# Optimization experiments

Hardware: AMD Instinct MI355X
Metric: run time of the kernel (lower is better)

Reference implementation:

```python
import jax, jax.numpy as jnp
import numpy as np

NUM_CARDS = 40
NUM_SUITS = 4
SIDE_SUIT_LEN = 9
NUM_ACTIONS = 2 * NUM_CARDS + 1  # 81 (use_signals=True)
NUM_TRICKS = 10


def setup_inputs() -> dict:
    key = jax.random.key(0)
    ks = jax.random.split(key, 8)
    B, A, D_in, D_q = 16384, 40, 4096, 256
    backbone_embed = jax.random.normal(ks[0], (B, D_in), dtype=jnp.float32)
    rank = jax.random.randint(ks[1], (B, A), -1, SIDE_SUIT_LEN)
    # guarantee at least one valid action per row (slot 0)
    rank = rank.at[:, 0].set(jnp.maximum(rank[:, 0], 0))
    suit = jax.random.randint(ks[2], (B, A), 0, NUM_SUITS + 1)  # suit==NUM_SUITS -> no-signal action
    valid_actions = jnp.stack([rank, suit], axis=-1)
    phase = jax.random.randint(ks[3], (B,), 0, 2)
    trick = jax.random.randint(ks[4], (B,), 0, NUM_TRICKS)
    # params
    Wq = jax.random.normal(ks[5], (D_in, D_q), dtype=jnp.float32) / np.sqrt(D_in).astype(np.float32)
    bq = jnp.zeros((D_q,), jnp.float32)
    key_table = jax.random.normal(ks[6], (NUM_ACTIONS, D_q), dtype=jnp.float32)
    ln_gamma = jnp.ones((D_q,), jnp.float32)
    ln_beta = jnp.zeros((D_q,), jnp.float32)
    # signal_prior == 'lin': p_signal = 2 / (num_tricks_left + 1)
    num_left = NUM_TRICKS - jnp.arange(NUM_TRICKS, dtype=jnp.float32)
    p_signal = 2.0 / (num_left + 1.0)
    return dict(backbone_embed=backbone_embed, valid_actions=valid_actions, phase=phase,
                trick=trick, Wq=Wq, bq=bq, key_table=key_table, ln_gamma=ln_gamma,
                ln_beta=ln_beta, p_signal=p_signal)


def reference(backbone_embed, valid_actions, phase, trick, Wq, bq, key_table, ln_gamma, ln_beta, p_signal):
    D_q = Wq.shape[1]
    rank = valid_actions[..., 0]          # (B, A)
    suit = valid_actions[..., 1]          # (B, A)
    aidx = phase[:, None] * NUM_CARDS + suit * SIDE_SUIT_LEN + rank
    aidx = jnp.where(rank == -1, -1, jnp.where(suit == NUM_SUITS, 2 * NUM_CARDS, aidx))
    # PaddedEmbed: shift by 1, row 0 is the zero padding row for idx == -1
    table = jnp.concatenate([jnp.zeros((1, D_q), key_table.dtype), key_table], axis=0)
    k = table[aidx + 1]                   # (B, A, D_q)
    # LayerNorm over last dim
    mu = k.mean(axis=-1, keepdims=True)
    var = k.var(axis=-1, keepdims=True)
    k = (k - mu) * jax.lax.rsqrt(var + 1e-5) * ln_gamma + ln_beta
    q = backbone_embed @ Wq + bq          # (B, D_q)
    attn = jnp.einsum('bq,baq->ba', q, k) / jnp.sqrt(jnp.float32(D_q))
    attn = jnp.where(rank == -1, -jnp.inf, attn)
    # no-signal bias on action 0 during signal phase
    n_valid = (rank != -1).sum(axis=-1).astype(jnp.float32)
    ps = p_signal[trick]
    w = jnp.log(jnp.maximum((1.0 - ps) / ps * (n_valid - 1.0), 1e-5))
    w = jnp.where(n_valid == 1.0, 0.0, w)
    attn = attn.at[:, 0].add(jnp.where(phase == 1, w, 0.0))
    return jax.nn.log_softmax(attn, axis=-1)
```

## Files before the change

### kernel.cpp

```cpp
#include <hip/hip_runtime.h>
#include <hip/hip_bf16.h>
#include <math.h>


typedef _Float16 half8_t __attribute__((ext_vector_type(8)));
typedef float    f32x4_t __attribute__((ext_vector_type(4)));

#define NUM_B 16384
#define D_IN  4096
#define D_Q   256
#define N_ACT 40

__device__ __forceinline__ half8_t cvt8(const float4 a, const float4 b) {
  half8_t h;
  h[0] = (_Float16)a.x; h[1] = (_Float16)a.y; h[2] = (_Float16)a.z; h[3] = (_Float16)a.w;
  h[4] = (_Float16)b.x; h[5] = (_Float16)b.y; h[6] = (_Float16)b.z; h[7] = (_Float16)b.w;
  return h;
}
__device__ __forceinline__ void gl_lds16f(const float* g, float* l) {
  __builtin_amdgcn_global_load_lds(
      (const __attribute__((address_space(1))) void*)g,
      (__attribute__((address_space(3))) void*)l, 16, 0, 0);
}
__device__ __forceinline__ void gl_lds16h(const _Float16* g, _Float16* l) {
  __builtin_amdgcn_global_load_lds(
      (const __attribute__((address_space(1))) void*)g,
      (__attribute__((address_space(3))) void*)l, 16, 0, 0);
}

__global__ __launch_bounds__(256) void ln_table_k(const float* __restrict__ kt,
                                                  const float* __restrict__ gamma,
                                                  const float* __restrict__ beta,
                                                  const float* __restrict__ bq,
                                                  float* __restrict__ out,
                                                  float* __restrict__ bqk) {
  __shared__ float red[8];
  __shared__ float red2[4];
  const int t = threadIdx.x, r = blockIdx.x;
  float v = kt[r * 256 + t];
  float s = v, sq = v * v;
#pragma unroll
  for (int off = 1; off < 64; off <<= 1) {
    s  += __shfl_xor(s, off);
    sq += __shfl_xor(sq, off);
  }
  if ((t & 63) == 0) { red[t >> 6] = s; red[4 + (t >> 6)] = sq; }
  __syncthreads();
  s  = red[0] + red[1] + red[2] + red[3];
  sq = red[4] + red[5] + red[6] + red[7];
  const float mu  = s * (1.0f / 256.0f);
  const float var = sq * (1.0f / 256.0f) - mu * mu;
  const float inv = 1.0f / sqrtf(var + 1e-5f);
  const float o = (v - mu) * inv * gamma[t] + beta[t];
  out[r * 256 + t] = o;
  float p = o * bq[t];
#pragma unroll
  for (int off = 1; off < 64; off <<= 1) p += __shfl_xor(p, off);
  if ((t & 63) == 0) red2[t >> 6] = p;
  __syncthreads();
  if (t == 0) bqk[r] = red2[0] + red2[1] + red2[2] + red2[3];
}

__global__ __launch_bounds__(256) void wk_gemm_k(const float* __restrict__ Wq,
                                                 const float* __restrict__ tbl,
                                                 _Float16* __restrict__ Bf) {
  const int lane = threadIdx.x & 63, w = threadIdx.x >> 6;
  const int wm = w >> 1, wn = w & 1;
  const int m0 = blockIdx.x * 64 + wm * 32;
  const int n0 = wn * 64;
  const int fr = lane & 15, fg = lane >> 4;
  f32x4_t acc[2][4] = {};
  for (int k0 = 0; k0 < 256; k0 += 32) {
    half8_t af[2], bf[4];
#pragma unroll
    for (int i = 0; i < 2; ++i) {
      const float* p = Wq + (size_t)(m0 + i * 16 + fr) * D_Q + k0 + fg * 8;
      af[i] = cvt8(*(const float4*)p, *(const float4*)(p + 4));
    }
#pragma unroll
    for (int j = 0; j < 4; ++j) {
      const int n = n0 + j * 16 + fr;
      if (n < 81) {
        const float* p = tbl + (size_t)n * D_Q + k0 + fg * 8;
        bf[j] = cvt8(*(const float4*)p, *(const float4*)(p + 4));
      } else {
        bf[j] = (half8_t)(_Float16)0.0f;
      }
    }
#pragma unroll
    for (int i = 0; i < 2; ++i)
#pragma unroll
      for (int j = 0; j < 4; ++j)
        acc[i][j] = __builtin_amdgcn_mfma_f32_16x16x32_f16(af[i], bf[j], acc[i][j], 0, 0, 0);
  }
#pragma unroll
  for (int i = 0; i < 2; ++i)
#pragma unroll
    for (int j = 0; j < 4; ++j)
#pragma unroll
      for (int r = 0; r < 4; ++r) {
        const int k = m0 + i * 16 + fg * 4 + r;
        const int n = n0 + j * 16 + fr;
        const int kt32 = k >> 5, fgb = (k >> 3) & 3, e = k & 7;
        const int jg = n >> 4, frb = n & 15;
        Bf[(((size_t)kt32 * 8 + jg) * 64 + fgb * 16 + frb) * 8 + e] =
            (_Float16)acc[i][j][r];
      }
}

__global__ __launch_bounds__(512) void gemm_part_k(const float* __restrict__ A,
                                                   const _Float16* __restrict__ Bf,
                                                   float* __restrict__ part) {
  __shared__ __align__(16) char smem[65536];
  float*    Afs = (float*)smem;
  _Float16* Bls = (_Float16*)(smem + 32768);

  const int t = threadIdx.x, lane = t & 63, w = t >> 6;
  const int fr = lane & 15, fg = lane >> 4;
  const int ks = blockIdx.y;
  const size_t row0 = (size_t)blockIdx.x * 64;
  const int k0 = ks * 2048;

#define STAGE(T, P)                                                           \
  do {                                                                        \
    float* abase = Afs + (P)*4096;                                            \
    _Float16* bbase = Bls + (P)*8192;                                         \
    _Pragma("unroll") for (int q_ = 0; q_ < 4; ++q_) {                        \
      const int id_ = w * 4 + q_;                                             \
      if (id_ < 16) {                                                         \
        const int r_ = id_ * 4 + (lane >> 4);                                 \
        gl_lds16f(A + (size_t)(row0 + r_) * D_IN + k0 + (T)*64 +              \
                      (((lane & 15) ^ (r_ & 7)) << 2),                        \
                  abase + id_ * 256);                                         \
      } else {                                                                \
        const int ib_ = id_ - 16;                                             \
        gl_lds16h(Bf + ((size_t)(ks * 32 + (T))) * 8192 + ib_ * 512 + lane * 8, \
                  bbase + ib_ * 512);                                         \
      }                                                                       \
    }                                                                         \
  } while (0)

  const int wm = w >> 2, wn = w & 3;
  int aoff[2][2][2], boff[2][2];
#pragma unroll
  for (int i = 0; i < 2; ++i)
#pragma unroll
    for (int c = 0; c < 2; ++c)
#pragma unroll
      for (int h = 0; h < 2; ++h)
        aoff[i][c][h] = (wm * 32 + i * 16 + fr) * 64 +
                        (((c * 8 + fg * 2 + h) ^ (fr & 7)) * 4);
#pragma unroll
  for (int c = 0; c < 2; ++c)
#pragma unroll
    for (int j = 0; j < 2; ++j)
      boff[c][j] = c * 4096 + (wn * 2 + j) * 512 + lane * 8;

  f32x4_t acc[2][2] = {};

  STAGE(0, 0);
  for (int kt = 0; kt < 32; ++kt) {
    if (kt < 31) STAGE(kt + 1, (kt + 1) & 1);
    __builtin_amdgcn_sched_barrier(0);
    if (kt < 31) asm volatile("s_waitcnt vmcnt(4)" ::: "memory");
    else         asm volatile("s_waitcnt vmcnt(0)" ::: "memory");
    __builtin_amdgcn_s_barrier();
    __builtin_amdgcn_sched_barrier(0);

    const float*    Ap = Afs + (kt & 1) * 4096;
    const _Float16* Bp = Bls + (kt & 1) * 8192;
#pragma unroll
    for (int c = 0; c < 2; ++c) {
      half8_t bfv[2];
#pragma unroll
      for (int j = 0; j < 2; ++j) bfv[j] = *(const half8_t*)(Bp + boff[c][j]);
#pragma unroll
      for (int i = 0; i < 2; ++i) {
        const float4 x0 = *(const float4*)(Ap + aoff[i][c][0]);
        const float4 x1 = *(const float4*)(Ap + aoff[i][c][1]);
        const half8_t af = cvt8(x0, x1);
#pragma unroll
        for (int j = 0; j < 2; ++j)
          acc[i][j] = __builtin_amdgcn_mfma_f32_16x16x32_f16(af, bfv[j], acc[i][j], 0, 0, 0);
      }
    }
    asm volatile("s_waitcnt lgkmcnt(0)" ::: "memory");
    __builtin_amdgcn_s_barrier();
    __builtin_amdgcn_sched_barrier(0);
  }
#undef STAGE

  float* pb = part + ((size_t)ks * NUM_B + row0) * 128;
#pragma unroll
  for (int i = 0; i < 2; ++i)
#pragma unroll
    for (int j = 0; j < 2; ++j) {
      const int col = wn * 32 + j * 16 + fr;
#pragma unroll
      for (int r = 0; r < 4; ++r)
        pb[(size_t)(wm * 32 + i * 16 + fg * 4 + r) * 128 + col] = acc[i][j][r];
    }
}

__global__ __launch_bounds__(256) void softmax_k(const float* __restrict__ part,
                                                 const float* __restrict__ bqk,
                                                 const int* __restrict__ va,
                                                 const int* __restrict__ phase,
                                                 const int* __restrict__ trick,
                                                 const float* __restrict__ psig,
                                                 float* __restrict__ out) {
  const int t = threadIdx.x;
  const int lane = t & 63, w = t >> 6;
  const int b = blockIdx.x * 4 + w;

  float sx = 0.f, sy = 0.f;
#pragma unroll
  for (int ks = 0; ks < 2; ++ks) {
    const float2 v = *(const float2*)&part[((size_t)ks * NUM_B + b) * 128 + lane * 2];
    sx += v.x; sy += v.y;
  }

  int rank = -1, suit = 0;
  if (lane < N_ACT) {
    rank = va[((size_t)b * N_ACT + lane) * 2];
    suit = va[((size_t)b * N_ACT + lane) * 2 + 1];
  }
  const int ph = phase[b];
  const bool valid = (rank >= 0);
  const int aidx = valid ? (suit == 4 ? 80 : ph * 40 + suit * 9 + rank) : -1;
  const int nvalid = __popcll(__ballot(valid));

  const int srcl = valid ? (aidx >> 1) : 0;
  const float v0 = __shfl(sx, srcl);
  const float v1 = __shfl(sy, srcl);

  float attn_l = -INFINITY;
  if (valid) attn_l = (((aidx & 1) ? v1 : v0) + bqk[aidx]) * 0.0625f;

  if (ph == 1 && lane == 0) {
    const float ps = psig[trick[b]];
    const float nv = (float)nvalid;
    const float wv = (nv == 1.0f) ? 0.0f
                                  : logf(fmaxf((1.0f - ps) / ps * (nv - 1.0f), 1e-5f));
    attn_l += wv;
  }

  float m = attn_l;
#pragma unroll
  for (int off = 1; off < 64; off <<= 1) m = fmaxf(m, __shfl_xor(m, off));
  const float e = expf(attn_l - m);
  float ssum = e;
#pragma unroll
  for (int off = 1; off < 64; off <<= 1) ssum += __shfl_xor(ssum, off);
  const float o = attn_l - m - logf(ssum);
  if (lane < N_ACT) out[(size_t)b * N_ACT + lane] = valid ? o : -3.0e38f;
}

extern "C" void kernel_launch(void* const* d_in, const int* in_sizes, int n_in,
                              void* d_out, int out_size, void* d_ws, size_t ws_size,
                              hipStream_t stream) {
  const float* backbone = (const float*)d_in[0];
  const int*   va       = (const int*)d_in[1];
  const int*   phase    = (const int*)d_in[2];
  const int*   trick    = (const int*)d_in[3];
  const float* Wq       = (const float*)d_in[4];
  const float* bq       = (const float*)d_in[5];
  const float* keytab   = (const float*)d_in[6];
  const float* gamma    = (const float*)d_in[7];
  const float* beta     = (const float*)d_in[8];
  const float* psig     = (const float*)d_in[9];
  float* out = (float*)d_out;

  char* ws = (char*)d_ws;
  _Float16* Bf   = (_Float16*)ws;
  float* tableLN = (float*)(ws + (1u << 20));
  float* bqk     = (float*)(ws + (1u << 20) + (128u << 10));
  float* part    = (float*)(ws + (2u << 20));

  ln_table_k<<<dim3(81), 256, 0, stream>>>(keytab, gamma, beta, bq, tableLN, bqk);
  wk_gemm_k<<<dim3(64), 256, 0, stream>>>(Wq, tableLN, Bf);
  gemm_part_k<<<dim3(NUM_B / 64, 2), 512, 0, stream>>>(backbone, Bf, part);
  softmax_k<<<dim3(NUM_B / 4), 256, 0, stream>>>(part, bqk, va, phase, trick,
                                                 psig, out);
}
```

Baseline: 89.68 us.

## Enlarge GEMM row tile to 128 and split K four ways

The query-key GEMM block now covers 128 rows instead of 64, and the K dimension is split into four partitions instead of two, keeping the same block count. A is staged 64 k-columns at a time, loaded in two halves across alternating iterations, while B is staged 32 k at a time. Each warp now owns a 32x64 output tile with 8 accumulators, so each staged B tile serves twice as many rows. The cost is double the partial-sum buffer traffic written by the GEMM and read by softmax, more LDS per block, and more complex vmcnt bookkeeping.

Result: slower. 105.2 us (+17.3%).

```diff
diff --git a/kernel.cpp b/kernel.cpp
--- a/kernel.cpp
+++ b/kernel.cpp
@@ -111,91 +111,100 @@
 __global__ __launch_bounds__(512) void gemm_part_k(const float* __restrict__ A,
                                                    const _Float16* __restrict__ Bf,
                                                    float* __restrict__ part) {
-  __shared__ __align__(16) char smem[65536];
+  __shared__ __align__(16) char smem[81920];
   float*    Afs = (float*)smem;
-  _Float16* Bls = (_Float16*)(smem + 32768);
+  _Float16* Bls = (_Float16*)(smem + 65536);
 
   const int t = threadIdx.x, lane = t & 63, w = t >> 6;
   const int fr = lane & 15, fg = lane >> 4;
   const int ks = blockIdx.y;
-  const size_t row0 = (size_t)blockIdx.x * 64;
-  const int k0 = ks * 2048;
-
-#define STAGE(T, P)                                                           \
+  const size_t row0 = (size_t)blockIdx.x * 128;
+  const int k0 = ks * 1024;
+
+#define STAGE_B(TB)                                                           \
   do {                                                                        \
-    float* abase = Afs + (P)*4096;                                            \
-    _Float16* bbase = Bls + (P)*8192;                                         \
-    _Pragma("unroll") for (int q_ = 0; q_ < 4; ++q_) {                        \
-      const int id_ = w * 4 + q_;                                             \
-      if (id_ < 16) {                                                         \
-        const int r_ = id_ * 4 + (lane >> 4);                                 \
-        gl_lds16f(A + (size_t)(row0 + r_) * D_IN + k0 + (T)*64 +              \
-                      (((lane & 15) ^ (r_ & 7)) << 2),                        \
-                  abase + id_ * 256);                                         \
-      } else {                                                                \
-        const int ib_ = id_ - 16;                                             \
-        gl_lds16h(Bf + ((size_t)(ks * 32 + (T))) * 8192 + ib_ * 512 + lane * 8, \
-                  bbase + ib_ * 512);                                         \
-      }                                                                       \
+    gl_lds16h(Bf + ((size_t)(ks * 32 + (TB))) * 4096 + w * 512 + lane * 8,    \
+              Bls + ((TB)&1) * 4096 + w * 512);                               \
+  } while (0)
+#define STAGE_A(SU, HF)                                                       \
+  do {                                                                        \
+    float* abase = Afs + ((SU)&1) * 8192;                                     \
+    _Pragma("unroll") for (int q_ = 0; q_ < 2; ++q_) {                        \
+      const int id_ = (HF)*16 + w * 2 + q_;                                   \
+      const int r_ = id_ * 4 + (lane >> 4);                                   \
+      gl_lds16f(A + (size_t)(row0 + r_) * D_IN + k0 + (SU)*64 +               \
+                    (((lane & 15) ^ (r_ & 7)) << 2),                          \
+                abase + id_ * 256);                                           \
     }                                                                         \
   } while (0)
 
-  const int wm = w >> 2, wn = w & 3;
-  int aoff[2][2][2], boff[2][2];
+  int aoff[2][2][2];
 #pragma unroll
   for (int i = 0; i < 2; ++i)
 #pragma unroll
-    for (int c = 0; c < 2; ++c)
-#pragma unroll
-      for (int h = 0; h < 2; ++h)
-        aoff[i][c][h] = (wm * 32 + i * 16 + fr) * 64 +
-                        (((c * 8 + fg * 2 + h) ^ (fr & 7)) * 4);
-#pragma unroll
-  for (int c = 0; c < 2; ++c)
-#pragma unroll
-    for (int j = 0; j < 2; ++j)
-      boff[c][j] = c * 4096 + (wn * 2 + j) * 512 + lane * 8;
-
-  f32x4_t acc[2][2] = {};
-
-  STAGE(0, 0);
+    for (int kh = 0; kh < 2; ++kh)
+#pragma unroll
+      for (int h = 0; h < 2; ++h) {
+        const int R = (w >> 1) * 32 + i * 16 + fr;
+        aoff[i][kh][h] = R * 64 + (((kh * 8 + fg * 2 + h) ^ (R & 7)) << 2);
+      }
+  const int wm = w >> 1, wn = w & 1;
+  int boff[4];
+#pragma unroll
+  for (int j = 0; j < 4; ++j) boff[j] = (wn * 4 + j) * 512 + lane * 8;
+
+  f32x4_t acc[2][4] = {};
+
+  STAGE_B(0);
+  STAGE_A(0, 0);
+  STAGE_A(0, 1);
+
   for (int kt = 0; kt < 32; ++kt) {
-    if (kt < 31) STAGE(kt + 1, (kt + 1) & 1);
+    if (kt < 31) STAGE_B(kt + 1);
+    if (kt < 30) {
+      if ((kt & 1) == 0) STAGE_A((kt >> 1) + 1, 0);
+      else               STAGE_A((kt >> 1) + 1, 1);
+    }
     __builtin_amdgcn_sched_barrier(0);
-    if (kt < 31) asm volatile("s_waitcnt vmcnt(4)" ::: "memory");
-    else         asm volatile("s_waitcnt vmcnt(0)" ::: "memory");
+    if (kt < 30) {
+      if ((kt & 1) == 0) asm volatile("s_waitcnt vmcnt(3)" ::: "memory");
+      else               asm volatile("s_waitcnt vmcnt(5)" ::: "memory");
+    } else if (kt == 30) {
+      asm volatile("s_waitcnt vmcnt(1)" ::: "memory");
+    } else {
+      asm volatile("s_waitcnt vmcnt(0)" ::: "memory");
+    }
     __builtin_amdgcn_s_barrier();
     __builtin_amdgcn_sched_barrier(0);
 
-    const float*    Ap = Afs + (kt & 1) * 4096;
-    const _Float16* Bp = Bls + (kt & 1) * 8192;
-#pragma unroll
-    for (int c = 0; c < 2; ++c) {
-      half8_t bfv[2];
-#pragma unroll
-      for (int j = 0; j < 2; ++j) bfv[j] = *(const half8_t*)(Bp + boff[c][j]);
-#pragma unroll
-      for (int i = 0; i < 2; ++i) {
-        const float4 x0 = *(const float4*)(Ap + aoff[i][c][0]);
-        const float4 x1 = *(const float4*)(Ap + aoff[i][c][1]);
-        const half8_t af = cvt8(x0, x1);
-#pragma unroll
-        for (int j = 0; j < 2; ++j)
-          acc[i][j] = __builtin_amdgcn_mfma_f32_16x16x32_f16(af, bfv[j], acc[i][j], 0, 0, 0);
-      }
+    const float*    Ap = Afs + ((kt >> 1) & 1) * 8192;
+    const _Float16* Bp = Bls + (kt & 1) * 4096;
+    const int kh = kt & 1;
+    half8_t bfv[4];
+#pragma unroll
+    for (int j = 0; j < 4; ++j) bfv[j] = *(const half8_t*)(Bp + boff[j]);
+#pragma unroll
+    for (int i = 0; i < 2; ++i) {
+      const float4 x0 = *(const float4*)(Ap + aoff[i][kh][0]);
+      const float4 x1 = *(const float4*)(Ap + aoff[i][kh][1]);
+      const half8_t af = cvt8(x0, x1);
+#pragma unroll
+      for (int j = 0; j < 4; ++j)
+        acc[i][j] = __builtin_amdgcn_mfma_f32_16x16x32_f16(af, bfv[j], acc[i][j], 0, 0, 0);
     }
     asm volatile("s_waitcnt lgkmcnt(0)" ::: "memory");
     __builtin_amdgcn_s_barrier();
     __builtin_amdgcn_sched_barrier(0);
   }
-#undef STAGE
+#undef STAGE_A
+#undef STAGE_B
 
   float* pb = part + ((size_t)ks * NUM_B + row0) * 128;
 #pragma unroll
   for (int i = 0; i < 2; ++i)
 #pragma unroll
-    for (int j = 0; j < 2; ++j) {
-      const int col = wn * 32 + j * 16 + fr;
+    for (int j = 0; j < 4; ++j) {
+      const int col = wn * 64 + j * 16 + fr;
 #pragma unroll
       for (int r = 0; r < 4; ++r)
         pb[(size_t)(wm * 32 + i * 16 + fg * 4 + r) * 128 + col] = acc[i][j][r];
@@ -215,7 +224,7 @@
 
   float sx = 0.f, sy = 0.f;
 #pragma unroll
-  for (int ks = 0; ks < 2; ++ks) {
+  for (int ks = 0; ks < 4; ++ks) {
     const float2 v = *(const float2*)&part[((size_t)ks * NUM_B + b) * 128 + lane * 2];
     sx += v.x; sy += v.y;
   }
@@ -279,7 +288,7 @@
 
   ln_table_k<<<dim3(81), 256, 0, stream>>>(keytab, gamma, beta, bq, tableLN, bqk);
   wk_gemm_k<<<dim3(64), 256, 0, stream>>>(Wq, tableLN, Bf);
-  gemm_part_k<<<dim3(NUM_B / 64, 2), 512, 0, stream>>>(backbone, Bf, part);
+  gemm_part_k<<<dim3(NUM_B / 128, 4), 512, 0, stream>>>(backbone, Bf, part);
   softmax_k<<<dim3(NUM_B / 4), 256, 0, stream>>>(part, bqk, va, phase, trick,
                                                  psig, out);
 }
```

## Use single-buffered 256-thread GEMM blocks with 4-way split-K for higher occupancy

Applied to the files above, without the earlier changes.

Reworks the main GEMM from 512-thread double-buffered blocks with 2-way split-K into 256-thread single-buffered blocks with 4-way split-K. Each warp now computes a 32x64 tile, and LDS per block drops to 32KB, so more blocks can be resident per CU. The aim is to hide memory latency through occupancy rather than explicit prefetch. In exchange, loads no longer overlap compute inside a block and two __syncthreads run per k-step. The partial-sum buffer also doubles, so the softmax kernel reads four partials instead of two.

Result: slower. 103.6 us (+15.5%).

```diff
diff --git a/kernel.cpp b/kernel.cpp
--- a/kernel.cpp
+++ b/kernel.cpp
@@ -108,85 +108,79 @@
       }
 }
 
-__global__ __launch_bounds__(512) void gemm_part_k(const float* __restrict__ A,
-                                                   const _Float16* __restrict__ Bf,
-                                                   float* __restrict__ part) {
-  __shared__ __align__(16) char smem[65536];
+__global__ __launch_bounds__(256, 4) void gemm_part_k(const float* __restrict__ A,
+                                                      const _Float16* __restrict__ Bf,
+                                                      float* __restrict__ part) {
+  __shared__ __align__(16) char smem[32768];
   float*    Afs = (float*)smem;
-  _Float16* Bls = (_Float16*)(smem + 32768);
+  _Float16* Bls = (_Float16*)(smem + 16384);
 
   const int t = threadIdx.x, lane = t & 63, w = t >> 6;
   const int fr = lane & 15, fg = lane >> 4;
   const int ks = blockIdx.y;
   const size_t row0 = (size_t)blockIdx.x * 64;
-  const int k0 = ks * 2048;
-
-#define STAGE(T, P)                                                           \
+  const int k0 = ks * 1024;
+
+#define STAGE(T)                                                              \
   do {                                                                        \
-    float* abase = Afs + (P)*4096;                                            \
-    _Float16* bbase = Bls + (P)*8192;                                         \
-    _Pragma("unroll") for (int q_ = 0; q_ < 4; ++q_) {                        \
-      const int id_ = w * 4 + q_;                                             \
+    _Pragma("unroll") for (int q_ = 0; q_ < 8; ++q_) {                        \
+      const int id_ = w * 8 + q_;                                             \
       if (id_ < 16) {                                                         \
         const int r_ = id_ * 4 + (lane >> 4);                                 \
         gl_lds16f(A + (size_t)(row0 + r_) * D_IN + k0 + (T)*64 +              \
                       (((lane & 15) ^ (r_ & 7)) << 2),                        \
-                  abase + id_ * 256);                                         \
+                  Afs + id_ * 256);                                           \
       } else {                                                                \
         const int ib_ = id_ - 16;                                             \
-        gl_lds16h(Bf + ((size_t)(ks * 32 + (T))) * 8192 + ib_ * 512 + lane * 8, \
-                  bbase + ib_ * 512);                                         \
+        gl_lds16h(Bf + ((size_t)(ks * 16 + (T))) * 8192 + ib_ * 512 + lane * 8, \
+                  Bls + ib_ * 512);                                           \
       }                                                                       \
     }                                                                         \
   } while (0)
 
-  const int wm = w >> 2, wn = w & 3;
-  int aoff[2][2][2], boff[2][2];
+  const int wm = w >> 1, wn = w & 1;
+  int aoff[2][2][2];
 #pragma unroll
   for (int i = 0; i < 2; ++i)
 #pragma unroll
     for (int c = 0; c < 2; ++c)
 #pragma unroll
-      for (int h = 0; h < 2; ++h)
-        aoff[i][c][h] = (wm * 32 + i * 16 + fr) * 64 +
-                        (((c * 8 + fg * 2 + h) ^ (fr & 7)) * 4);
+      for (int h = 0; h < 2; ++h) {
+        const int R = wm * 32 + i * 16 + fr;
+        aoff[i][c][h] = R * 64 + (((c * 8 + fg * 2 + h) ^ (R & 7)) << 2);
+      }
+  int boff[2][4];
 #pragma unroll
   for (int c = 0; c < 2; ++c)
 #pragma unroll
-    for (int j = 0; j < 2; ++j)
-      boff[c][j] = c * 4096 + (wn * 2 + j) * 512 + lane * 8;
-
-  f32x4_t acc[2][2] = {};
-
-  STAGE(0, 0);
-  for (int kt = 0; kt < 32; ++kt) {
-    if (kt < 31) STAGE(kt + 1, (kt + 1) & 1);
-    __builtin_amdgcn_sched_barrier(0);
-    if (kt < 31) asm volatile("s_waitcnt vmcnt(4)" ::: "memory");
-    else         asm volatile("s_waitcnt vmcnt(0)" ::: "memory");
-    __builtin_amdgcn_s_barrier();
-    __builtin_amdgcn_sched_barrier(0);
-
-    const float*    Ap = Afs + (kt & 1) * 4096;
-    const _Float16* Bp = Bls + (kt & 1) * 8192;
+    for (int j = 0; j < 4; ++j)
+      boff[c][j] = c * 4096 + (wn * 4 + j) * 512 + lane * 8;
+
+  f32x4_t acc[2][4] = {};
+
+  STAGE(0);
+  __syncthreads();
+  for (int kt = 0; kt < 16; ++kt) {
 #pragma unroll
     for (int c = 0; c < 2; ++c) {
-      half8_t bfv[2];
-#pragma unroll
-      for (int j = 0; j < 2; ++j) bfv[j] = *(const half8_t*)(Bp + boff[c][j]);
+      half8_t bfv[4];
+#pragma unroll
+      for (int j = 0; j < 4; ++j) bfv[j] = *(const half8_t*)(Bls + boff[c][j]);
 #pragma unroll
       for (int i = 0; i < 2; ++i) {
-        const float4 x0 = *(const float4*)(Ap + aoff[i][c][0]);
-        const float4 x1 = *(const float4*)(Ap + aoff[i][c][1]);
+        const float4 x0 = *(const float4*)(Afs + aoff[i][c][0]);
+        const float4 x1 = *(const float4*)(Afs + aoff[i][c][1]);
         const half8_t af = cvt8(x0, x1);
 #pragma unroll
-        for (int j = 0; j < 2; ++j)
+        for (int j = 0; j < 4; ++j)
           acc[i][j] = __builtin_amdgcn_mfma_f32_16x16x32_f16(af, bfv[j], acc[i][j], 0, 0, 0);
       }
     }
-    asm volatile("s_waitcnt lgkmcnt(0)" ::: "memory");
-    __builtin_amdgcn_s_barrier();
-    __builtin_amdgcn_sched_barrier(0);
+    if (kt < 15) {
+      __syncthreads();
+      STAGE(kt + 1);
+      __syncthreads();
+    }
   }
 #undef STAGE
 
@@ -194,8 +188,8 @@
 #pragma unroll
   for (int i = 0; i < 2; ++i)
 #pragma unroll
-    for (int j = 0; j < 2; ++j) {
-      const int col = wn * 32 + j * 16 + fr;
+    for (int j = 0; j < 4; ++j) {
+      const int col = wn * 64 + j * 16 + fr;
 #pragma unroll
       for (int r = 0; r < 4; ++r)
         pb[(size_t)(wm * 32 + i * 16 + fg * 4 + r) * 128 + col] = acc[i][j][r];
@@ -215,7 +209,7 @@
 
   float sx = 0.f, sy = 0.f;
 #pragma unroll
-  for (int ks = 0; ks < 2; ++ks) {
+  for (int ks = 0; ks < 4; ++ks) {
     const float2 v = *(const float2*)&part[((size_t)ks * NUM_B + b) * 128 + lane * 2];
     sx += v.x; sy += v.y;
   }
@@ -279,7 +273,7 @@
 
   ln_table_k<<<dim3(81), 256, 0, stream>>>(keytab, gamma, beta, bq, tableLN, bqk);
   wk_gemm_k<<<dim3(64), 256, 0, stream>>>(Wq, tableLN, Bf);
-  gemm_part_k<<<dim3(NUM_B / 64, 2), 512, 0, stream>>>(backbone, Bf, part);
+  gemm_part_k<<<dim3(NUM_B / 64, 4), 256, 0, stream>>>(backbone, Bf, part);
   softmax_k<<<dim3(NUM_B / 4), 256, 0, stream>>>(part, bqk, va, phase, trick,
                                                  psig, out);
 }
```

## Pad folded key matrix to 96 columns instead of 128 in GEMM

Applied to the files above, without the earlier changes.

Shrinks the padded N dimension of the folded Wq·key_table matrix from 128 to 96 columns, which covers the 81 actions with less padding. The main GEMM drops the now-unneeded MFMAs, moves less B data per stage and writes smaller partial outputs. The softmax kernel reads the correspondingly smaller partials. Warp roles are reorganized so 4 waves load A and 4 load B, with per-role vmcnt waits, which adds some load-balance asymmetry.

Result: faster. 83.93 us (median of 2 runs) (-6.4%).

```diff
diff --git a/kernel.cpp b/kernel.cpp
--- a/kernel.cpp
+++ b/kernel.cpp
@@ -10,6 +10,7 @@
 #define D_IN  4096
 #define D_Q   256
 #define N_ACT 40
+#define NPAD  96
 
 __device__ __forceinline__ half8_t cvt8(const float4 a, const float4 b) {
   half8_t h;
@@ -67,18 +68,18 @@
   const int lane = threadIdx.x & 63, w = threadIdx.x >> 6;
   const int wm = w >> 1, wn = w & 1;
   const int m0 = blockIdx.x * 64 + wm * 32;
-  const int n0 = wn * 64;
+  const int n0 = wn * 48;
   const int fr = lane & 15, fg = lane >> 4;
-  f32x4_t acc[2][4] = {};
+  f32x4_t acc[2][3] = {};
   for (int k0 = 0; k0 < 256; k0 += 32) {
-    half8_t af[2], bf[4];
+    half8_t af[2], bf[3];
 #pragma unroll
     for (int i = 0; i < 2; ++i) {
       const float* p = Wq + (size_t)(m0 + i * 16 + fr) * D_Q + k0 + fg * 8;
       af[i] = cvt8(*(const float4*)p, *(const float4*)(p + 4));
     }
 #pragma unroll
-    for (int j = 0; j < 4; ++j) {
+    for (int j = 0; j < 3; ++j) {
       const int n = n0 + j * 16 + fr;
       if (n < 81) {
         const float* p = tbl + (size_t)n * D_Q + k0 + fg * 8;
@@ -90,20 +91,19 @@
 #pragma unroll
     for (int i = 0; i < 2; ++i)
 #pragma unroll
-      for (int j = 0; j < 4; ++j)
+      for (int j = 0; j < 3; ++j)
         acc[i][j] = __builtin_amdgcn_mfma_f32_16x16x32_f16(af[i], bf[j], acc[i][j], 0, 0, 0);
   }
 #pragma unroll
   for (int i = 0; i < 2; ++i)
 #pragma unroll
-    for (int j = 0; j < 4; ++j)
+    for (int j = 0; j < 3; ++j)
 #pragma unroll
       for (int r = 0; r < 4; ++r) {
         const int k = m0 + i * 16 + fg * 4 + r;
         const int n = n0 + j * 16 + fr;
-        const int kt32 = k >> 5, fgb = (k >> 3) & 3, e = k & 7;
-        const int jg = n >> 4, frb = n & 15;
-        Bf[(((size_t)kt32 * 8 + jg) * 64 + fgb * 16 + frb) * 8 + e] =
+        Bf[(((size_t)(k >> 5) * 6 + (n >> 4)) * 64 +
+            (((k >> 3) & 3) * 16 + (n & 15))) * 8 + (k & 7)] =
             (_Float16)acc[i][j][r];
       }
 }
@@ -111,7 +111,7 @@
 __global__ __launch_bounds__(512) void gemm_part_k(const float* __restrict__ A,
                                                    const _Float16* __restrict__ Bf,
                                                    float* __restrict__ part) {
-  __shared__ __align__(16) char smem[65536];
+  __shared__ __align__(16) char smem[57344];
   float*    Afs = (float*)smem;
   _Float16* Bls = (_Float16*)(smem + 32768);
 
@@ -123,66 +123,70 @@
 
 #define STAGE(T, P)                                                           \
   do {                                                                        \
-    float* abase = Afs + (P)*4096;                                            \
-    _Float16* bbase = Bls + (P)*8192;                                         \
-    _Pragma("unroll") for (int q_ = 0; q_ < 4; ++q_) {                        \
-      const int id_ = w * 4 + q_;                                             \
-      if (id_ < 16) {                                                         \
+    if (w < 4) {                                                              \
+      float* abase = Afs + (P)*4096;                                          \
+      _Pragma("unroll") for (int q_ = 0; q_ < 4; ++q_) {                      \
+        const int id_ = w * 4 + q_;                                           \
         const int r_ = id_ * 4 + (lane >> 4);                                 \
         gl_lds16f(A + (size_t)(row0 + r_) * D_IN + k0 + (T)*64 +              \
                       (((lane & 15) ^ (r_ & 7)) << 2),                        \
                   abase + id_ * 256);                                         \
-      } else {                                                                \
-        const int ib_ = id_ - 16;                                             \
-        gl_lds16h(Bf + ((size_t)(ks * 32 + (T))) * 8192 + ib_ * 512 + lane * 8, \
+      }                                                                       \
+    } else {                                                                  \
+      _Float16* bbase = Bls + (P)*6144;                                       \
+      _Pragma("unroll") for (int q_ = 0; q_ < 3; ++q_) {                      \
+        const int ib_ = (w - 4) * 3 + q_;                                     \
+        gl_lds16h(Bf + ((size_t)(ks * 64 + (T)*2 + (ib_ / 6)) * 6 +           \
+                        (ib_ % 6)) * 512 + lane * 8,                          \
                   bbase + ib_ * 512);                                         \
       }                                                                       \
     }                                                                         \
   } while (0)
 
-  const int wm = w >> 2, wn = w & 3;
-  int aoff[2][2][2], boff[2][2];
-#pragma unroll
-  for (int i = 0; i < 2; ++i)
-#pragma unroll
-    for (int c = 0; c < 2; ++c)
-#pragma unroll
-      for (int h = 0; h < 2; ++h)
-        aoff[i][c][h] = (wm * 32 + i * 16 + fr) * 64 +
-                        (((c * 8 + fg * 2 + h) ^ (fr & 7)) * 4);
+  const int wm = w >> 1, wn = w & 1;
+  int aoff[2][2];
 #pragma unroll
   for (int c = 0; c < 2; ++c)
 #pragma unroll
-    for (int j = 0; j < 2; ++j)
-      boff[c][j] = c * 4096 + (wn * 2 + j) * 512 + lane * 8;
-
-  f32x4_t acc[2][2] = {};
+    for (int h = 0; h < 2; ++h) {
+      const int R = wm * 16 + fr;
+      aoff[c][h] = R * 64 + (((c * 8 + fg * 2 + h) ^ (R & 7)) << 2);
+    }
+  int boff[2][3];
+#pragma unroll
+  for (int c = 0; c < 2; ++c)
+#pragma unroll
+    for (int j = 0; j < 3; ++j)
+      boff[c][j] = c * 3072 + (wn * 3 + j) * 512 + lane * 8;
+
+  f32x4_t acc[3] = {};
 
   STAGE(0, 0);
   for (int kt = 0; kt < 32; ++kt) {
     if (kt < 31) STAGE(kt + 1, (kt + 1) & 1);
     __builtin_amdgcn_sched_barrier(0);
-    if (kt < 31) asm volatile("s_waitcnt vmcnt(4)" ::: "memory");
-    else         asm volatile("s_waitcnt vmcnt(0)" ::: "memory");
+    if (kt < 31) {
+      if (w < 4) asm volatile("s_waitcnt vmcnt(4)" ::: "memory");
+      else       asm volatile("s_waitcnt vmcnt(3)" ::: "memory");
+    } else {
+      asm volatile("s_waitcnt vmcnt(0)" ::: "memory");
+    }
     __builtin_amdgcn_s_barrier();
     __builtin_amdgcn_sched_barrier(0);
 
     const float*    Ap = Afs + (kt & 1) * 4096;
-    const _Float16* Bp = Bls + (kt & 1) * 8192;
+    const _Float16* Bp = Bls + (kt & 1) * 6144;
 #pragma unroll
     for (int c = 0; c < 2; ++c) {
-      half8_t bfv[2];
-#pragma unroll
-      for (int j = 0; j < 2; ++j) bfv[j] = *(const half8_t*)(Bp + boff[c][j]);
-#pragma unroll
-      for (int i = 0; i < 2; ++i) {
-        const float4 x0 = *(const float4*)(Ap + aoff[i][c][0]);
-        const float4 x1 = *(const float4*)(Ap + aoff[i][c][1]);
-        const half8_t af = cvt8(x0, x1);
-#pragma unroll
-        for (int j = 0; j < 2; ++j)
-          acc[i][j] = __builtin_amdgcn_mfma_f32_16x16x32_f16(af, bfv[j], acc[i][j], 0, 0, 0);
-      }
+      half8_t bfv[3];
+#pragma unroll
+      for (int j = 0; j < 3; ++j) bfv[j] = *(const half8_t*)(Bp + boff[c][j]);
+      const float4 x0 = *(const float4*)(Ap + aoff[c][0]);
+      const float4 x1 = *(const float4*)(Ap + aoff[c][1]);
+      const half8_t af = cvt8(x0, x1);
+#pragma unroll
+      for (int j = 0; j < 3; ++j)
+        acc[j] = __builtin_amdgcn_mfma_f32_16x16x32_f16(af, bfv[j], acc[j], 0, 0, 0);
     }
     asm volatile("s_waitcnt lgkmcnt(0)" ::: "memory");
     __builtin_amdgcn_s_barrier();
@@ -190,16 +194,14 @@
   }
 #undef STAGE
 
-  float* pb = part + ((size_t)ks * NUM_B + row0) * 128;
-#pragma unroll
-  for (int i = 0; i < 2; ++i)
-#pragma unroll
-    for (int j = 0; j < 2; ++j) {
-      const int col = wn * 32 + j * 16 + fr;
-#pragma unroll
-      for (int r = 0; r < 4; ++r)
-        pb[(size_t)(wm * 32 + i * 16 + fg * 4 + r) * 128 + col] = acc[i][j][r];
-    }
+  float* pb = part + ((size_t)ks * NUM_B + row0) * NPAD;
+#pragma unroll
+  for (int j = 0; j < 3; ++j) {
+    const int col = wn * 48 + j * 16 + fr;
+#pragma unroll
+    for (int r = 0; r < 4; ++r)
+      pb[(size_t)(wm * 16 + fg * 4 + r) * NPAD + col] = acc[j][r];
+  }
 }
 
 __global__ __launch_bounds__(256) void softmax_k(const float* __restrict__ part,
@@ -214,10 +216,12 @@
   const int b = blockIdx.x * 4 + w;
 
   float sx = 0.f, sy = 0.f;
-#pragma unroll
-  for (int ks = 0; ks < 2; ++ks) {
-    const float2 v = *(const float2*)&part[((size_t)ks * NUM_B + b) * 128 + lane * 2];
-    sx += v.x; sy += v.y;
+  if (lane < 48) {
+#pragma unroll
+    for (int ks = 0; ks < 2; ++ks) {
+      const float2 v = *(const float2*)&part[((size_t)ks * NUM_B + b) * NPAD + lane * 2];
+      sx += v.x; sy += v.y;
+    }
   }
 
   int rank = -1, suit = 0;
```
